# Kernel tuning notes

Measured on AMD Instinct MI355X. Metric: run time of the kernel, lower is better.

## Reference

```python
import jax, jax.numpy as jnp
import numpy as np

N = 262144      # nodes per graph
NC = 65536      # common nodes
D = 256         # feature_dim


def setup_inputs() -> dict:
    key = jax.random.key(0)
    ks = jax.random.split(key, 12)
    h_prop = jax.random.normal(ks[0], (N, D), dtype=jnp.float32)
    h_context = jax.random.normal(ks[1], (N, D), dtype=jnp.float32)
    h_orig = jax.random.normal(ks[2], (NC, D), dtype=jnp.float32)
    # unique indices (torch scatter-assign semantics are only well-defined without dups)
    idx_prop = jnp.sort(jax.random.permutation(ks[3], N)[:NC]).astype(jnp.int64)
    idx_ctx = jnp.sort(jax.random.permutation(ks[4], N)[:NC]).astype(jnp.int64)
    # parameters (xavier-ish scale)
    s = 1.0 / np.sqrt(D)
    w_orig = jax.random.normal(ks[5], (D, D), dtype=jnp.float32) * s
    w_prop = jax.random.normal(ks[6], (D, D), dtype=jnp.float32) * s
    w_ctx = jax.random.normal(ks[7], (D, D), dtype=jnp.float32) * s
    W_fuse = jax.random.normal(ks[8], (D, 3 * D), dtype=jnp.float32) * (1.0 / np.sqrt(3 * D))  # torch Linear weight (out,in)
    b_fuse = jnp.zeros((D,), dtype=jnp.float32)
    bias = jax.random.uniform(ks[9], (D,), dtype=jnp.float32, minval=-s, maxval=s)
    return {
        "h_prop": h_prop, "h_context": h_context,
        "h_original_common_nodes": h_orig,
        "w_orig": w_orig, "w_prop": w_prop, "w_ctx": w_ctx,
        "W_fuse": W_fuse, "b_fuse": b_fuse, "bias": bias,
        "common_node_indices_in_prop": idx_prop,
        "common_node_indices_in_context": idx_ctx,
    }


def reference(h_prop, h_context, h_original_common_nodes,
              w_orig, w_prop, w_ctx, W_fuse, b_fuse, bias,
              common_node_indices_in_prop, common_node_indices_in_context):
    # gather common rows + three small GEMMs  [NC, D]
    t_orig = h_original_common_nodes @ w_orig
    t_prop = h_prop[common_node_indices_in_prop] @ w_prop
    t_ctx = h_context[common_node_indices_in_context] @ w_ctx
    # concat-linear-tanh-bias  [NC, D]
    fused = jnp.concatenate([t_orig, t_prop, t_ctx], axis=1) @ W_fuse.T + b_fuse
    fused = jnp.tanh(fused) + bias
    # scatter update into clones of the full tables
    h_prop_updated = h_prop.at[common_node_indices_in_prop].set(fused)
    h_context_updated = h_context.at[common_node_indices_in_context].set(fused)
    return (h_prop_updated, h_context_updated)
```

## Files before the change

### kernel.cpp

```cpp
#include <hip/hip_runtime.h>
#include <hip/hip_bf16.h>
#include <math.h>

#define NN 262144
#define NCC 65536

typedef __bf16 bf16x8 __attribute__((ext_vector_type(8)));
typedef __bf16 bf16x4 __attribute__((ext_vector_type(4)));
typedef float f32x4 __attribute__((ext_vector_type(4)));

__global__ __launch_bounds__(256) void k_setup(const float* __restrict__ w_orig,
                                               const float* __restrict__ w_prop,
                                               const float* __restrict__ w_ctx,
                                               const float* __restrict__ W_fuse,
                                               __bf16* __restrict__ Mt,
                                               unsigned char* __restrict__ flags) {
    __shared__ float Wl[64 * 65];
    __shared__ float wl[64 * 65];
    int b = blockIdx.x;
    int t = threadIdx.x;
    if (b >= 48) {
        ((uint4*)flags)[(b - 48) * 256 + t] = make_uint4(0u, 0u, 0u, 0u);
        return;
    }
    int seg = b >> 4, rem = b & 15;
    int ot = rem >> 2, mt = rem & 3;
    const float* wseg = seg == 0 ? w_orig : (seg == 1 ? w_prop : w_ctx);
    int to = (t & 15) * 4, tm = (t >> 4) * 4;
    float acc[4][4] = {};
    for (int kc = 0; kc < 4; ++kc) {
        __syncthreads();
        for (int i = 0; i < 16; ++i) {
            int f = i * 256 + t;
            int row = f >> 6, col = f & 63;
            Wl[row * 65 + col] = W_fuse[(size_t)(ot * 64 + row) * 768 + seg * 256 + kc * 64 + col];
            wl[row * 65 + col] = wseg[(size_t)(mt * 64 + row) * 256 + kc * 64 + col];
        }
        __syncthreads();
        for (int k = 0; k < 64; ++k) {
            float wo[4], wm2[4];
#pragma unroll
            for (int i = 0; i < 4; ++i) wo[i] = Wl[(to + i) * 65 + k];
#pragma unroll
            for (int j = 0; j < 4; ++j) wm2[j] = wl[(tm + j) * 65 + k];
#pragma unroll
            for (int i = 0; i < 4; ++i)
#pragma unroll
                for (int j = 0; j < 4; ++j) acc[i][j] += wo[i] * wm2[j];
        }
    }
    for (int i = 0; i < 4; ++i)
        for (int j = 0; j < 4; ++j) {
            int o = ot * 64 + to + i;
            int g = seg * 256 + mt * 64 + tm + j;
            Mt[(size_t)o * 768 + g] = (__bf16)acc[i][j];
        }
}

__global__ void k_setflags(const int* __restrict__ idxp, const int* __restrict__ idxc,
                           unsigned char* fp, unsigned char* fc) {
    int j = blockIdx.x * blockDim.x + threadIdx.x;
    if (j < NCC) { fp[idxp[j]] = 1; fc[idxc[j]] = 1; }
}

#define MFMA __builtin_amdgcn_mfma_f32_16x16x32_bf16

__global__ __launch_bounds__(512, 4) void k_main(const float* __restrict__ hp,
                                                 const float* __restrict__ hc,
                                                 const float* __restrict__ horig,
                                                 const __bf16* __restrict__ Mt,
                                                 const float* __restrict__ bfuse,
                                                 const float* __restrict__ bias,
                                                 const int* __restrict__ idxp,
                                                 const int* __restrict__ idxc,
                                                 const unsigned char* __restrict__ fp,
                                                 const unsigned char* __restrict__ fc,
                                                 float* __restrict__ out0,
                                                 float* __restrict__ out1) {
    __shared__ __align__(16) char smem[32768];
    int bid = blockIdx.x >> 1;
    int t = threadIdx.x;

    if (!(blockIdx.x & 1)) {
        int tbl = bid >= 512;
        const unsigned char* F = tbl ? fc : fp;
        const float* S = tbl ? hc : hp;
        float* D = tbl ? out1 : out0;
        int r0 = (tbl ? bid - 512 : bid) * 512;
#pragma unroll
        for (int g = 0; g < 8; ++g) {
            unsigned char fl[8];
            f32x4 v[8];
#pragma unroll
            for (int i = 0; i < 8; ++i) {
                int gl = (g * 8 + i) * 512 + t;
                fl[i] = F[r0 + (gl >> 6)];
            }
#pragma unroll
            for (int i = 0; i < 8; ++i) {
                int gl = (g * 8 + i) * 512 + t;
                int r = r0 + (gl >> 6), slot = gl & 63;
                v[i] = *(const f32x4*)(S + (size_t)(fl[i] ? 0 : r) * 256 + slot * 4);
            }
#pragma unroll
            for (int i = 0; i < 8; ++i) {
                int gl = (g * 8 + i) * 512 + t;
                int r = r0 + (gl >> 6), slot = gl & 63;
                if (!fl[i]) *(f32x4*)(D + (size_t)r * 256 + slot * 4) = v[i];
            }
        }
        return;
    }

    int jbase = bid * 64;
    int lane = t & 63, wid = t >> 6;
    int wm = wid >> 2, wn = wid & 3;
    int l15 = lane & 15, lq = lane >> 4;

    const __bf16* bp[4];
#pragma unroll
    for (int ni = 0; ni < 4; ++ni)
        bp[ni] = Mt + (size_t)(wn * 64 + ni * 16 + l15) * 768 + lq * 8;

    f32x4 acc[2][4] = {};

    f32x4 v[8];
#pragma unroll
    for (int i = 0; i < 8; ++i)
        v[i] = *(const f32x4*)(horig + (size_t)(jbase + wid * 8 + i) * 256 + lane * 4);

#pragma unroll
    for (int seg = 0; seg < 3; ++seg) {
        bf16x4 w[8];
#pragma unroll
        for (int i = 0; i < 8; ++i) {
            w[i][0] = (__bf16)v[i][0]; w[i][1] = (__bf16)v[i][1];
            w[i][2] = (__bf16)v[i][2]; w[i][3] = (__bf16)v[i][3];
        }
        __syncthreads();
#pragma unroll
        for (int i = 0; i < 8; ++i) {
            int r = wid * 8 + i;
            *(bf16x4*)(smem + r * 512 + ((lane * 8) ^ ((r & 7) << 4))) = w[i];
        }
        if (seg < 2) {
#pragma unroll
            for (int i = 0; i < 8; ++i) {
                int j = jbase + wid * 8 + i;
                const float* src = (seg == 0) ? hp + (size_t)idxp[j] * 256
                                              : hc + (size_t)idxc[j] * 256;
                v[i] = *(const f32x4*)(src + lane * 4);
            }
        }
        __syncthreads();
#pragma unroll
        for (int c = 0; c < 4; ++c) {
            int cg = seg * 4 + c;
            bf16x8 bfr[4][2];
#pragma unroll
            for (int ni = 0; ni < 4; ++ni)
#pragma unroll
                for (int ks = 0; ks < 2; ++ks)
                    bfr[ni][ks] = *(const bf16x8*)(bp[ni] + cg * 64 + ks * 32);
            bf16x8 af[2][2];
#pragma unroll
            for (int mi = 0; mi < 2; ++mi)
#pragma unroll
                for (int ks = 0; ks < 2; ++ks) {
                    int row = wm * 32 + mi * 16 + l15;
                    int boff = (c * 128 + ks * 64 + lq * 16) ^ ((row & 7) << 4);
                    af[mi][ks] = *(const bf16x8*)(smem + row * 512 + boff);
                }
#pragma unroll
            for (int ks = 0; ks < 2; ++ks)
#pragma unroll
                for (int mi = 0; mi < 2; ++mi)
#pragma unroll
                    for (int ni = 0; ni < 4; ++ni)
                        acc[mi][ni] = MFMA(af[mi][ks], bfr[ni][ks], acc[mi][ni], 0, 0, 0);
        }
    }

    float bfv[4], biv[4];
#pragma unroll
    for (int ni = 0; ni < 4; ++ni) {
        int o = wn * 64 + ni * 16 + l15;
        bfv[ni] = bfuse[o];
        biv[ni] = bias[o];
    }
    __syncthreads();
    float* scr = (float*)(smem + wid * 4096);
#pragma unroll
    for (int mi = 0; mi < 2; ++mi) {
#pragma unroll
        for (int ni = 0; ni < 4; ++ni)
#pragma unroll
            for (int rr = 0; rr < 4; ++rr) {
                float v2 = tanhf(acc[mi][ni][rr] + bfv[ni]) + biv[ni];
                scr[(lq * 4 + rr) * 64 + ni * 16 + l15] = v2;
            }
#pragma unroll
        for (int rnd = 0; rnd < 4; ++rnd) {
            int rr2 = rnd * 4 + lq;
            int j = jbase + wm * 32 + mi * 16 + rr2;
            int gp = idxp[j], gc = idxc[j];
            f32x4 vv = *(const f32x4*)&scr[rr2 * 64 + l15 * 4];
            *(f32x4*)(out0 + (size_t)gp * 256 + wn * 64 + l15 * 4) = vv;
            *(f32x4*)(out1 + (size_t)gc * 256 + wn * 64 + l15 * 4) = vv;
        }
    }
}

extern "C" void kernel_launch(void* const* d_in, const int* in_sizes, int n_in,
                              void* d_out, int out_size, void* d_ws, size_t ws_size,
                              hipStream_t stream) {
    const float* hp     = (const float*)d_in[0];
    const float* hc     = (const float*)d_in[1];
    const float* horig  = (const float*)d_in[2];
    const float* w_orig = (const float*)d_in[3];
    const float* w_prop = (const float*)d_in[4];
    const float* w_ctx  = (const float*)d_in[5];
    const float* W_fuse = (const float*)d_in[6];
    const float* bfuse  = (const float*)d_in[7];
    const float* bias   = (const float*)d_in[8];
    const int* idxp     = (const int*)d_in[9];
    const int* idxc     = (const int*)d_in[10];
    float* out0 = (float*)d_out;
    float* out1 = out0 + (size_t)NN * 256;

    char* ws = (char*)d_ws;
    __bf16* Mt = (__bf16*)ws;
    unsigned char* fp = (unsigned char*)(ws + 393216);
    unsigned char* fc = fp + NN;

    k_setup<<<176, 256, 0, stream>>>(w_orig, w_prop, w_ctx, W_fuse, Mt, fp);
    k_setflags<<<NCC / 256, 256, 0, stream>>>(idxp, idxc, fp, fc);
    k_main<<<2048, 512, 0, stream>>>(hp, hc, horig, Mt, bfuse, bias,
                                     idxp, idxc, fp, fc, out0, out1);
}
```

Before: 352.0 us.

## Stage fused weight tiles through LDS with register prefetch and restructured epilogue

The B operand (the fused bf16 weight matrix) was read directly from global memory by each wave. It is now cooperatively loaded into a swizzled LDS buffer per k-chunk, with the next chunk prefetched into registers. The A tile layout is changed to per-chunk 8 KB slabs, and gather indices are loaded once into registers. The epilogue writes full rows through LDS so each wave stores whole 1 KB rows to the scattered outputs. LDS doubles to 64 KB and the syncthreads calls become raw barriers, which adds barriers per chunk and may reduce occupancy.

After: 297.4 us. 1.18x faster.

```diff
diff --git a/kernel.cpp b/kernel.cpp
--- a/kernel.cpp
+++ b/kernel.cpp
@@ -8,6 +8,10 @@
 typedef __bf16 bf16x8 __attribute__((ext_vector_type(8)));
 typedef __bf16 bf16x4 __attribute__((ext_vector_type(4)));
 typedef float f32x4 __attribute__((ext_vector_type(4)));
+
+#define RAW_BARRIER() __builtin_amdgcn_s_barrier()
+#define LGKM0() asm volatile("s_waitcnt lgkmcnt(0)" ::: "memory")
+#define MFMA __builtin_amdgcn_mfma_f32_16x16x32_bf16
 
 __global__ __launch_bounds__(256) void k_setup(const float* __restrict__ w_orig,
                                                const float* __restrict__ w_prop,
@@ -63,8 +67,6 @@
     if (j < NCC) { fp[idxp[j]] = 1; fc[idxc[j]] = 1; }
 }
 
-#define MFMA __builtin_amdgcn_mfma_f32_16x16x32_bf16
-
 __global__ __launch_bounds__(512, 4) void k_main(const float* __restrict__ hp,
                                                  const float* __restrict__ hc,
                                                  const float* __restrict__ horig,
@@ -77,7 +79,7 @@
                                                  const unsigned char* __restrict__ fc,
                                                  float* __restrict__ out0,
                                                  float* __restrict__ out1) {
-    __shared__ __align__(16) char smem[32768];
+    __shared__ __align__(16) char smem[65536];
     int bid = blockIdx.x >> 1;
     int t = threadIdx.x;
 
@@ -112,72 +114,90 @@
         return;
     }
 
+    __bf16* Bl = (__bf16*)(smem + 32768);
     int jbase = bid * 64;
     int lane = t & 63, wid = t >> 6;
     int wm = wid >> 2, wn = wid & 3;
     int l15 = lane & 15, lq = lane >> 4;
 
-    const __bf16* bp[4];
-#pragma unroll
-    for (int ni = 0; ni < 4; ++ni)
-        bp[ni] = Mt + (size_t)(wn * 64 + ni * 16 + l15) * 768 + lq * 8;
-
-    f32x4 acc[2][4] = {};
+    int ip[8], ic[8];
+#pragma unroll
+    for (int i = 0; i < 8; ++i) {
+        int j = jbase + wid * 8 + i;
+        ip[i] = idxp[j];
+        ic[i] = idxc[j];
+    }
+
+    int bo = t >> 1, bkp = t & 1;
+    const __bf16* bsrc = Mt + (size_t)bo * 768 + bkp * 32;
 
     f32x4 v[8];
 #pragma unroll
     for (int i = 0; i < 8; ++i)
         v[i] = *(const f32x4*)(horig + (size_t)(jbase + wid * 8 + i) * 256 + lane * 4);
+    bf16x8 vb[4];
+#pragma unroll
+    for (int i = 0; i < 4; ++i) vb[i] = *(const bf16x8*)(bsrc + i * 8);
+
+    f32x4 acc[2][4] = {};
+
+    int acb = (lane >> 4) * 8192;
+    int as8 = l15 >> 1;
+    int ahb = (lane & 1) * 8;
 
 #pragma unroll
     for (int seg = 0; seg < 3; ++seg) {
-        bf16x4 w[8];
-#pragma unroll
-        for (int i = 0; i < 8; ++i) {
-            w[i][0] = (__bf16)v[i][0]; w[i][1] = (__bf16)v[i][1];
-            w[i][2] = (__bf16)v[i][2]; w[i][3] = (__bf16)v[i][3];
-        }
-        __syncthreads();
+        RAW_BARRIER();
 #pragma unroll
         for (int i = 0; i < 8; ++i) {
             int r = wid * 8 + i;
-            *(bf16x4*)(smem + r * 512 + ((lane * 8) ^ ((r & 7) << 4))) = w[i];
+            bf16x4 w;
+            w[0] = (__bf16)v[i][0]; w[1] = (__bf16)v[i][1];
+            w[2] = (__bf16)v[i][2]; w[3] = (__bf16)v[i][3];
+            *(bf16x4*)(smem + acb + r * 128 + (((as8 ^ (r & 7)) << 4)) + ahb) = w;
         }
         if (seg < 2) {
 #pragma unroll
             for (int i = 0; i < 8; ++i) {
-                int j = jbase + wid * 8 + i;
-                const float* src = (seg == 0) ? hp + (size_t)idxp[j] * 256
-                                              : hc + (size_t)idxc[j] * 256;
+                const float* src = (seg == 0) ? hp + (size_t)ip[i] * 256 : hc + (size_t)ic[i] * 256;
                 v[i] = *(const f32x4*)(src + lane * 4);
             }
         }
-        __syncthreads();
 #pragma unroll
         for (int c = 0; c < 4; ++c) {
             int cg = seg * 4 + c;
-            bf16x8 bfr[4][2];
-#pragma unroll
-            for (int ni = 0; ni < 4; ++ni)
-#pragma unroll
-                for (int ks = 0; ks < 2; ++ks)
-                    bfr[ni][ks] = *(const bf16x8*)(bp[ni] + cg * 64 + ks * 32);
-            bf16x8 af[2][2];
-#pragma unroll
-            for (int mi = 0; mi < 2; ++mi)
-#pragma unroll
-                for (int ks = 0; ks < 2; ++ks) {
-                    int row = wm * 32 + mi * 16 + l15;
-                    int boff = (c * 128 + ks * 64 + lq * 16) ^ ((row & 7) << 4);
-                    af[mi][ks] = *(const bf16x8*)(smem + row * 512 + boff);
+            if (c) RAW_BARRIER();
+#pragma unroll
+            for (int i = 0; i < 4; ++i) {
+                int slot = bkp * 4 + i;
+                *(bf16x8*)&Bl[bo * 64 + ((slot ^ (bo & 7)) << 3)] = vb[i];
+            }
+            if (cg < 11) {
+#pragma unroll
+                for (int i = 0; i < 4; ++i) vb[i] = *(const bf16x8*)(bsrc + (cg + 1) * 64 + i * 8);
+            }
+            LGKM0();
+            RAW_BARRIER();
+#pragma unroll
+            for (int ks = 0; ks < 2; ++ks) {
+                bf16x8 af[2], bfr[4];
+                int kslot = ks * 4 + lq;
+#pragma unroll
+                for (int mi = 0; mi < 2; ++mi) {
+                    int r = wm * 32 + mi * 16 + l15;
+                    af[mi] = *(const bf16x8*)(smem + c * 8192 + r * 128 + ((kslot ^ (r & 7)) << 4));
                 }
 #pragma unroll
-            for (int ks = 0; ks < 2; ++ks)
+                for (int ni = 0; ni < 4; ++ni) {
+                    int o = wn * 64 + ni * 16 + l15;
+                    bfr[ni] = *(const bf16x8*)&Bl[o * 64 + ((kslot ^ (o & 7)) << 3)];
+                }
 #pragma unroll
                 for (int mi = 0; mi < 2; ++mi)
 #pragma unroll
                     for (int ni = 0; ni < 4; ++ni)
-                        acc[mi][ni] = MFMA(af[mi][ks], bfr[ni][ks], acc[mi][ni], 0, 0, 0);
+                        acc[mi][ni] = MFMA(af[mi], bfr[ni], acc[mi][ni], 0, 0, 0);
+            }
         }
     }
 
@@ -188,26 +208,27 @@
         bfv[ni] = bfuse[o];
         biv[ni] = bias[o];
     }
-    __syncthreads();
-    float* scr = (float*)(smem + wid * 4096);
-#pragma unroll
-    for (int mi = 0; mi < 2; ++mi) {
+    LGKM0();
+    RAW_BARRIER();
+    float* scr = (float*)smem;
+#pragma unroll
+    for (int mi = 0; mi < 2; ++mi)
 #pragma unroll
         for (int ni = 0; ni < 4; ++ni)
 #pragma unroll
             for (int rr = 0; rr < 4; ++rr) {
-                float v2 = tanhf(acc[mi][ni][rr] + bfv[ni]) + biv[ni];
-                scr[(lq * 4 + rr) * 64 + ni * 16 + l15] = v2;
-            }
-#pragma unroll
-        for (int rnd = 0; rnd < 4; ++rnd) {
-            int rr2 = rnd * 4 + lq;
-            int j = jbase + wm * 32 + mi * 16 + rr2;
-            int gp = idxp[j], gc = idxc[j];
-            f32x4 vv = *(const f32x4*)&scr[rr2 * 64 + l15 * 4];
-            *(f32x4*)(out0 + (size_t)gp * 256 + wn * 64 + l15 * 4) = vv;
-            *(f32x4*)(out1 + (size_t)gc * 256 + wn * 64 + l15 * 4) = vv;
-        }
+                float val = tanhf(acc[mi][ni][rr] + bfv[ni]) + biv[ni];
+                int jr2 = wm * 32 + mi * 16 + lq * 4 + rr;
+                scr[jr2 * 256 + wn * 64 + ni * 16 + l15] = val;
+            }
+    LGKM0();
+    RAW_BARRIER();
+#pragma unroll
+    for (int i = 0; i < 8; ++i) {
+        int jj = wid * 8 + i;
+        f32x4 val = *(const f32x4*)(smem + jj * 1024 + lane * 16);
+        *(f32x4*)(out0 + (size_t)ip[i] * 256 + lane * 4) = val;
+        *(f32x4*)(out1 + (size_t)ic[i] * 256 + lane * 4) = val;
     }
 }
 
```
